# Optimization experiments

Measured on AMD Instinct MI355X. Metric: run time of the kernel, lower is better.

## Reference

```python
import jax, jax.numpy as jnp
import numpy as np

NUM_HEADS = 16
HEAD_DIM = 64
SCALE = 1.0 / np.sqrt(HEAD_DIM).astype(np.float32)


def _clinear(xr, xi, wr, wi):
    # complex matmul: (xr + i xi) @ (wr + i wi)
    yr = jnp.dot(xr, wr) - jnp.dot(xi, wi)
    yi = jnp.dot(xr, wi) + jnp.dot(xi, wr)
    return yr, yi


def setup_inputs() -> dict:
    key = jax.random.key(0)
    ks = jax.random.split(key, 12)
    B, L, S, C = 2, 2048, 2048, 1024
    glorot = 1.0 / np.sqrt(C)
    inp = {
        'inputs_real': jax.random.normal(ks[0], (B, L, C), jnp.float32),
        'inputs_imag': jax.random.normal(ks[1], (B, L, C), jnp.float32),
        'context_real': jax.random.normal(ks[2], (B, S, C), jnp.float32),
        'context_imag': jax.random.normal(ks[3], (B, S, C), jnp.float32),
        'wq_r': jax.random.normal(ks[4], (C, C), jnp.float32) * glorot,
        'wq_i': jax.random.normal(ks[5], (C, C), jnp.float32) * glorot,
        'wk_r': jax.random.normal(ks[6], (C, C), jnp.float32) * glorot,
        'wk_i': jax.random.normal(ks[7], (C, C), jnp.float32) * glorot,
        'wv_r': jax.random.normal(ks[8], (C, C), jnp.float32) * glorot,
        'wv_i': jax.random.normal(ks[9], (C, C), jnp.float32) * glorot,
        'wo_r': jax.random.normal(ks[10], (C, C), jnp.float32) * glorot,
        'wo_i': jax.random.normal(ks[11], (C, C), jnp.float32) * glorot,
        'bo_r': jnp.zeros((C,), jnp.float32),
        'bo_i': jnp.zeros((C,), jnp.float32),
    }
    return inp


def reference(inputs_real, inputs_imag, context_real, context_imag,
              wq_r, wq_i, wk_r, wk_i, wv_r, wv_i, wo_r, wo_i, bo_r, bo_i):
    B, L, C = inputs_real.shape
    S = context_real.shape[1]
    H, D = NUM_HEADS, HEAD_DIM

    qr, qi = _clinear(inputs_real, inputs_imag, wq_r, wq_i)
    kr, ki = _clinear(context_real, context_imag, wk_r, wk_i)
    vr, vi = _clinear(context_real, context_imag, wv_r, wv_i)

    qr = qr.reshape(B, L, H, D); qi = qi.reshape(B, L, H, D)
    kr = kr.reshape(B, S, H, D); ki = ki.reshape(B, S, H, D)
    vr = vr.reshape(B, S, H, D); vi = vi.reshape(B, S, H, D)

    # real part of q . conj-free inner product: qr.kr + qi.ki, scaled
    scores = (jnp.einsum('blhd,bshd->bhls', qr, kr)
              + jnp.einsum('blhd,bshd->bhls', qi, ki)) * SCALE
    attn = jax.nn.softmax(scores, axis=-1)

    out_r = jnp.einsum('bhls,bshd->blhd', attn, vr).reshape(B, L, C)
    out_i = jnp.einsum('bhls,bshd->blhd', attn, vi).reshape(B, L, C)

    yr, yi = _clinear(out_r, out_i, wo_r, wo_i)
    yr = yr + bo_r
    yi = yi + bo_i
    # stack real/imag parts: shape [2, B, L, C]
    return jnp.stack([yr, yi], axis=0)
```

## Files before the change

kernel.cpp:

```cpp
#include <hip/hip_runtime.h>

#define BB 2
#define LQ 2048
#define SK 2048
#define CH 1024
#define NH 16
#define HD 64
#define GK 2048
#define MM 4096
#define ATT_SCALE 0.125f

typedef _Float16 f16x8 __attribute__((ext_vector_type(8)));
typedef float f32x4 __attribute__((ext_vector_type(4)));
typedef unsigned short u16x8 __attribute__((ext_vector_type(8)));

__device__ __forceinline__ unsigned short h2u(_Float16 h) {
    union { _Float16 h; unsigned short u; } v; v.h = h; return v.u;
}
__device__ __forceinline__ void gload16(const _Float16* g, unsigned short* l) {
    __builtin_amdgcn_global_load_lds(
        (const __attribute__((address_space(1))) void*)g,
        (__attribute__((address_space(3))) void*)l, 16, 0, 0);
}

__device__ __forceinline__ float dpp_max16(float x) {
    union { float f; int i; } v, r;
    v.f = x;
    r.i = __builtin_amdgcn_update_dpp(v.i, v.i, 0xB1, 0xF, 0xF, false);
    v.f = fmaxf(v.f, r.f);
    r.i = __builtin_amdgcn_update_dpp(v.i, v.i, 0x4E, 0xF, 0xF, false);
    v.f = fmaxf(v.f, r.f);
    r.i = __builtin_amdgcn_update_dpp(v.i, v.i, 0x141, 0xF, 0xF, false);
    v.f = fmaxf(v.f, r.f);
    r.i = __builtin_amdgcn_update_dpp(v.i, v.i, 0x140, 0xF, 0xF, false);
    v.f = fmaxf(v.f, r.f);
    return v.f;
}

struct PackXEnt { const float* r; const float* i; _Float16* dst; };
struct PackXBatch { PackXEnt e[2]; };

__global__ __launch_bounds__(256) void pack_x_kernel(PackXBatch b)
{
    PackXEnt e = b.e[blockIdx.z];
    const size_t total = (size_t)MM * GK;
    for (size_t idx = (size_t)blockIdx.x * 256 + threadIdx.x; idx < total;
         idx += (size_t)gridDim.x * 256) {
        size_t m = idx >> 11;
        int c = (int)(idx & 2047);
        float v = (c < CH) ? e.r[m * CH + c] : e.i[m * CH + (c - CH)];
        e.dst[idx] = (_Float16)v;
    }
}

struct PackWEnt { const float* a; const float* b; float signb; _Float16* dst; };
struct PackWBatch { PackWEnt e[8]; };

__global__ __launch_bounds__(256) void pack_w_kernel(PackWBatch bt)
{
    PackWEnt e = bt.e[blockIdx.z];
    const int k0 = blockIdx.x * 32;
    const int n0 = blockIdx.y * 32;
    const float* src = (k0 < CH) ? e.a : e.b;
    const float sign = (k0 < CH) ? 1.f : e.signb;
    const int kk = k0 & (CH - 1);

    __shared__ float sT[32][33];
    const int t = threadIdx.x;
    const int tx = t & 31, ty = t >> 5;

    #pragma unroll
    for (int r = 0; r < 4; r++) {
        int kl = ty + r * 8;
        sT[kl][tx] = src[(size_t)(kk + kl) * CH + n0 + tx] * sign;
    }
    __syncthreads();
    #pragma unroll
    for (int r = 0; r < 4; r++) {
        int nl = ty + r * 8;
        e.dst[(size_t)(n0 + nl) * GK + k0 + tx] = (_Float16)sT[tx][nl];
    }
}

struct GemmEnt { const _Float16* A; const _Float16* Bt; void* out;
                 const float* bias; int mode; int part; };
struct GemmBatch { GemmEnt e[6]; };

#define NT   (GK / 32)
#define BUFH 12288

#define SWZ(x) ((x) ^ ((((x) >> 7) & 3) << 4))

__global__ __launch_bounds__(512, 2) void mfma_cgemm(GemmBatch bt)
{
    GemmEnt e = bt.e[blockIdx.z];
    __shared__ unsigned short lds[4 * BUFH];

    const int t    = threadIdx.x;
    const int wave = t >> 6;
    const int lane = t & 63;
    const int lm   = lane & 15;
    const int quad = lane >> 4;
    const int wr   = wave >> 1;
    const int wc   = wave & 1;

    const int m0 = blockIdx.y * 256;
    const int n0 = blockIdx.x * 128;

    int srow[2], scol[2];
    #pragma unroll
    for (int L = 0; L < 2; L++) {
        int p = (L * 512 + t) * 16;
        int q = SWZ(p);
        srow[L] = q >> 6;
        scol[L] = (q >> 1) & 31;
    }

    const _Float16* gA = e.A  + (size_t)m0 * GK;
    const _Float16* gB = e.Bt + (size_t)n0 * GK;

    auto stage = [&](int kt) {
        unsigned short* base = lds + (kt & 3) * BUFH;
        #pragma unroll
        for (int L = 0; L < 2; L++)
            gload16(gA + (size_t)srow[L] * GK + kt * 32 + scol[L],
                    base + (L * 512 + t) * 8);
        gload16(gB + (size_t)srow[0] * GK + kt * 32 + scol[0],
                base + 8192 + t * 8);
    };

    const int qA    = (wr * 64 + lm) * 64 + quad * 16;
    const int physA = SWZ(qA) >> 1;
    const int qB    = (wc * 64 + lm) * 64 + quad * 16;
    const int physB = (SWZ(qB) >> 1) + 8192;

    f32x4 acc[4][4] = {};

    stage(0); stage(1); stage(2);
    asm volatile("s_waitcnt vmcnt(6)" ::: "memory");
    __builtin_amdgcn_s_barrier();

    for (int kt = 0; kt < NT; ++kt) {
        const unsigned short* buf = lds + (kt & 3) * BUFH;
        f16x8 af[4], bf[4];
        #pragma unroll
        for (int i = 0; i < 4; i++)
            af[i] = *(const f16x8*)&buf[physA + i * 512];
        #pragma unroll
        for (int j = 0; j < 4; j++)
            bf[j] = *(const f16x8*)&buf[physB + j * 512];

        if (kt + 3 < NT) stage(kt + 3);

        __builtin_amdgcn_s_barrier();
        asm volatile("s_waitcnt lgkmcnt(0)" ::: "memory");
        __builtin_amdgcn_s_setprio(1);
        #pragma unroll
        for (int i = 0; i < 4; i++)
            #pragma unroll
            for (int j = 0; j < 4; j++)
                acc[i][j] = __builtin_amdgcn_mfma_f32_16x16x32_f16(
                    af[i], bf[j], acc[i][j], 0, 0, 0);
        __builtin_amdgcn_s_setprio(0);

        if (kt < NT - 3)       asm volatile("s_waitcnt vmcnt(6)" ::: "memory");
        else if (kt == NT - 3) asm volatile("s_waitcnt vmcnt(3)" ::: "memory");
        else if (kt == NT - 2) asm volatile("s_waitcnt vmcnt(0)" ::: "memory");
        __builtin_amdgcn_s_barrier();
    }

    const int mode = e.mode, part = e.part;
    #pragma unroll
    for (int j = 0; j < 4; j++) {
        int gcol = n0 + wc * 64 + j * 16 + lm;
        float bv = (mode == 2 && e.bias) ? e.bias[gcol] : 0.f;
        #pragma unroll
        for (int i = 0; i < 4; i++) {
            int growb = m0 + wr * 64 + i * 16 + quad * 4;
            #pragma unroll
            for (int reg = 0; reg < 4; reg++) {
                int grow = growb + reg;
                float v = acc[i][j][reg];
                if (mode == 2) {
                    ((float*)e.out)[(size_t)grow * CH + gcol] = v + bv;
                } else {
                    int b = grow >> 11, l = grow & 2047;
                    int h = gcol >> 6, dd = gcol & 63;
                    size_t off;
                    if (mode == 0)
                        off = (((size_t)(b * NH + h)) * LQ + l) * 128 + part * 64 + dd;
                    else
                        off = (((size_t)(b * NH + h)) * 128 + part * 64 + dd) * SK + l;
                    ((_Float16*)e.out)[off] = (_Float16)v;
                }
            }
        }
    }
}

#define KSTR 136
#define PSTR 72

__global__ __launch_bounds__(256, 2) void attn_mfma(
    const _Float16* __restrict__ Qp, const _Float16* __restrict__ Kp,
    const _Float16* __restrict__ Vt, _Float16* __restrict__ Aattn)
{
    __shared__ unsigned short lds[28288];
    unsigned short* sP = lds;
    unsigned short* sK = lds + 9216;
    unsigned short* sV = lds + 17920;

    const int t    = threadIdx.x;
    const int w    = t >> 6;
    const int lane = t & 63;
    const int lm   = lane & 15;
    const int quad = lane >> 4;

    const int bid = blockIdx.x;
    const int mt  = bid & 15;
    const int h   = (bid >> 4) & 15;
    const int b   = bid >> 8;

    const _Float16* qb = Qp + (((size_t)(b * NH + h)) * LQ + (size_t)mt * 128) * 128;
    const _Float16* kb = Kp + ((size_t)(b * NH + h)) * SK * 128;
    const _Float16* vb = Vt + ((size_t)(b * NH + h)) * 128 * SK;

    #pragma unroll
    for (int p = 0; p < 8; p++) {
        int idx = p * 256 + t;
        int r = idx >> 4, sg = idx & 15;
        *(u16x8*)&lds[r * KSTR + sg * 8] = *(const u16x8*)(qb + (size_t)r * 128 + sg * 8);
    }
    for (int idx = t; idx < 16 * PSTR; idx += 256) {
        sV[128 * PSTR + idx] = 0x3C00;
    }
    __syncthreads();

    f16x8 qf[2][4];
    #pragma unroll
    for (int i = 0; i < 2; i++)
        #pragma unroll
        for (int kk = 0; kk < 4; kk++)
            qf[i][kk] = *(const f16x8*)&lds[(w * 32 + i * 16 + lm) * KSTR + kk * 32 + quad * 8];

    u16x8 kreg[4], vreg[4];
    #pragma unroll
    for (int p = 0; p < 4; p++) {
        int idx = p * 256 + t;
        int r = idx >> 4, sg = idx & 15;
        kreg[p] = *(const u16x8*)(kb + (size_t)r * 128 + sg * 8);
        int rv = idx >> 3, sv = idx & 7;
        vreg[p] = *(const u16x8*)(vb + (size_t)rv * SK + sv * 8);
    }

    f32x4 oacc[2][9] = {};
    float m_st[2][4];
    #pragma unroll
    for (int i = 0; i < 2; i++)
        #pragma unroll
        for (int r = 0; r < 4; r++) m_st[i][r] = -1e30f;

    const float SC2 = ATT_SCALE * 1.44269504f;

    for (int it = 0; it < SK / 64; ++it) {
        __syncthreads();
        #pragma unroll
        for (int p = 0; p < 4; p++) {
            int idx = p * 256 + t;
            int r = idx >> 4, sg = idx & 15;
            *(u16x8*)&sK[r * KSTR + sg * 8] = kreg[p];
            int rv = idx >> 3, sv = idx & 7;
            *(u16x8*)&sV[rv * PSTR + sv * 8] = vreg[p];
        }
        __syncthreads();

        if (it + 1 < SK / 64) {
            int s0n = (it + 1) * 64;
            #pragma unroll
            for (int p = 0; p < 4; p++) {
                int idx = p * 256 + t;
                int r = idx >> 4, sg = idx & 15;
                kreg[p] = *(const u16x8*)(kb + (size_t)(s0n + r) * 128 + sg * 8);
                int rv = idx >> 3, sv = idx & 7;
                vreg[p] = *(const u16x8*)(vb + (size_t)rv * SK + s0n + sv * 8);
            }
        }

        f32x4 sacc[2][4] = {};
        #pragma unroll
        for (int kk = 0; kk < 4; kk++) {
            f16x8 bfr[4];
            #pragma unroll
            for (int j = 0; j < 4; j++)
                bfr[j] = *(const f16x8*)&sK[(j * 16 + lm) * KSTR + kk * 32 + quad * 8];
            #pragma unroll
            for (int i = 0; i < 2; i++)
                #pragma unroll
                for (int j = 0; j < 4; j++)
                    sacc[i][j] = __builtin_amdgcn_mfma_f32_16x16x32_f16(
                        qf[i][kk], bfr[j], sacc[i][j], 0, 0, 0);
        }

        #pragma unroll
        for (int i = 0; i < 2; i++) {
            #pragma unroll
            for (int r = 0; r < 4; r++) {
                float mx = fmaxf(fmaxf(sacc[i][0][r], sacc[i][1][r]),
                                 fmaxf(sacc[i][2][r], sacc[i][3][r]));
                mx = dpp_max16(mx) * SC2;
                float mnew = fmaxf(m_st[i][r], mx);
                float al = exp2f(m_st[i][r] - mnew);
                m_st[i][r] = mnew;
                int prow = (w * 32 + i * 16 + quad * 4 + r) * PSTR;
                #pragma unroll
                for (int j = 0; j < 4; j++) {
                    float p = exp2f(sacc[i][j][r] * SC2 - mnew);
                    sP[prow + j * 16 + lm] = h2u((_Float16)p);
                }
                #pragma unroll
                for (int j2 = 0; j2 < 9; j2++)
                    oacc[i][j2][r] *= al;
            }
        }

        #pragma unroll
        for (int kk = 0; kk < 2; kk++) {
            f16x8 pf[2], vf[9];
            #pragma unroll
            for (int i = 0; i < 2; i++)
                pf[i] = *(const f16x8*)&sP[(w * 32 + i * 16 + lm) * PSTR + kk * 32 + quad * 8];
            #pragma unroll
            for (int j2 = 0; j2 < 9; j2++)
                vf[j2] = *(const f16x8*)&sV[(j2 * 16 + lm) * PSTR + kk * 32 + quad * 8];
            #pragma unroll
            for (int i = 0; i < 2; i++)
                #pragma unroll
                for (int j2 = 0; j2 < 9; j2++)
                    oacc[i][j2] = __builtin_amdgcn_mfma_f32_16x16x32_f16(
                        pf[i], vf[j2], oacc[i][j2], 0, 0, 0);
        }
    }

    #pragma unroll
    for (int i = 0; i < 2; i++) {
        #pragma unroll
        for (int r = 0; r < 4; r++) {
            float inv = 1.f / oacc[i][8][r];
            int ml = w * 32 + i * 16 + quad * 4 + r;
            size_t row = (size_t)b * LQ + (size_t)mt * 128 + ml;
            #pragma unroll
            for (int j2 = 0; j2 < 8; j2++) {
                int d = j2 * 16 + lm;
                int dcol = (d < HD) ? h * HD + d : CH + h * HD + (d - HD);
                Aattn[row * GK + dcol] = (_Float16)(oacc[i][j2][r] * inv);
            }
        }
    }
}

extern "C" void kernel_launch(void* const* d_in, const int* in_sizes, int n_in,
                              void* d_out, int out_size, void* d_ws, size_t ws_size,
                              hipStream_t stream)
{
    const float* in_r = (const float*)d_in[0];
    const float* in_i = (const float*)d_in[1];
    const float* cx_r = (const float*)d_in[2];
    const float* cx_i = (const float*)d_in[3];
    const float* wq_r = (const float*)d_in[4];
    const float* wq_i = (const float*)d_in[5];
    const float* wk_r = (const float*)d_in[6];
    const float* wk_i = (const float*)d_in[7];
    const float* wv_r = (const float*)d_in[8];
    const float* wv_i = (const float*)d_in[9];
    const float* wo_r = (const float*)d_in[10];
    const float* wo_i = (const float*)d_in[11];
    const float* bo_r = (const float*)d_in[12];
    const float* bo_i = (const float*)d_in[13];

    _Float16* ws = (_Float16*)d_ws;
    const size_t A_ELEMS = (size_t)MM * GK;
    const size_t B_ELEMS = (size_t)CH * GK;
    const size_t H_ELEMS = (size_t)BB * NH * LQ * 128;

    _Float16* Ain   = ws;
    _Float16* Aattn = ws;
    _Float16* Actx  = Ain + A_ELEMS;
    _Float16* Bp    = Actx + A_ELEMS;
    _Float16* Qp    = Bp + 8 * B_ELEMS;
    _Float16* Kp    = Qp + H_ELEMS;
    _Float16* Vt    = Kp + H_ELEMS;

    _Float16* Bq_r = Bp + 0 * B_ELEMS;
    _Float16* Bq_i = Bp + 1 * B_ELEMS;
    _Float16* Bk_r = Bp + 2 * B_ELEMS;
    _Float16* Bk_i = Bp + 3 * B_ELEMS;
    _Float16* Bv_r = Bp + 4 * B_ELEMS;
    _Float16* Bv_i = Bp + 5 * B_ELEMS;
    _Float16* Bo_r = Bp + 6 * B_ELEMS;
    _Float16* Bo_i = Bp + 7 * B_ELEMS;

    float* out = (float*)d_out;
    float* yr = out;
    float* yi = out + (size_t)MM * CH;

    PackXBatch px;
    px.e[0] = { in_r, in_i, Ain  };
    px.e[1] = { cx_r, cx_i, Actx };
    pack_x_kernel<<<dim3(4096, 1, 2), 256, 0, stream>>>(px);

    PackWBatch pw;
    pw.e[0] = { wq_r, wq_i, -1.f, Bq_r };
    pw.e[1] = { wq_i, wq_r,  1.f, Bq_i };
    pw.e[2] = { wk_r, wk_i, -1.f, Bk_r };
    pw.e[3] = { wk_i, wk_r,  1.f, Bk_i };
    pw.e[4] = { wv_r, wv_i, -1.f, Bv_r };
    pw.e[5] = { wv_i, wv_r,  1.f, Bv_i };
    pw.e[6] = { wo_r, wo_i, -1.f, Bo_r };
    pw.e[7] = { wo_i, wo_r,  1.f, Bo_i };
    pack_w_kernel<<<dim3(GK / 32, CH / 32, 8), 256, 0, stream>>>(pw);

    GemmBatch gq;
    gq.e[0] = { Ain,  Bq_r, Qp, nullptr, 0, 0 };
    gq.e[1] = { Ain,  Bq_i, Qp, nullptr, 0, 1 };
    gq.e[2] = { Actx, Bk_r, Kp, nullptr, 0, 0 };
    gq.e[3] = { Actx, Bk_i, Kp, nullptr, 0, 1 };
    gq.e[4] = { Actx, Bv_r, Vt, nullptr, 1, 0 };
    gq.e[5] = { Actx, Bv_i, Vt, nullptr, 1, 1 };
    mfma_cgemm<<<dim3(CH / 128, MM / 256, 6), 512, 0, stream>>>(gq);

    attn_mfma<<<dim3(BB * NH * (LQ / 128)), 256, 0, stream>>>(Qp, Kp, Vt, Aattn);

    GemmBatch go;
    go.e[0] = { Aattn, Bo_r, yr, bo_r, 2, 0 };
    go.e[1] = { Aattn, Bo_i, yi, bo_i, 2, 1 };
    for (int z = 2; z < 6; z++) go.e[z] = go.e[0];
    mfma_cgemm<<<dim3(CH / 128, MM / 256, 2), 512, 0, stream>>>(go);
}
```

Baseline: 486.7 us.

## Swizzle attention LDS layout, remap block order, and add lazy softmax rescaling

Padded LDS strides for Q, K, V and P are replaced by an XOR swizzle. This shrinks the shared buffer and is meant to avoid bank conflicts on the MFMA fragment reads. Block indices are remapped so consecutive workgroups spread across heads/batches, presumably to balance work across XCDs and their caches. The online softmax now rescales the output accumulators only when the running max grows by more than 8 in the log2 domain. This skips most rescale multiplies, at the risk of fp16 P values reaching up to 2^8 before normalization.

```diff
diff --git a/kernel.cpp b/kernel.cpp
--- a/kernel.cpp
+++ b/kernel.cpp
@@ -35,6 +35,10 @@
     r.i = __builtin_amdgcn_update_dpp(v.i, v.i, 0x140, 0xF, 0xF, false);
     v.f = fmaxf(v.f, r.f);
     return v.f;
+}
+
+__device__ __forceinline__ int swzi(int row, int colh, int ldh) {
+    return row * ldh + (colh ^ ((row & 7) << 3));
 }
 
 struct PackXEnt { const float* r; const float* i; _Float16* dst; };
@@ -198,17 +202,14 @@
     }
 }
 
-#define KSTR 136
-#define PSTR 72
-
 __global__ __launch_bounds__(256, 2) void attn_mfma(
     const _Float16* __restrict__ Qp, const _Float16* __restrict__ Kp,
     const _Float16* __restrict__ Vt, _Float16* __restrict__ Aattn)
 {
-    __shared__ unsigned short lds[28288];
+    __shared__ unsigned short lds[25600];
     unsigned short* sP = lds;
-    unsigned short* sK = lds + 9216;
-    unsigned short* sV = lds + 17920;
+    unsigned short* sK = lds + 8192;
+    unsigned short* sV = lds + 16384;
 
     const int t    = threadIdx.x;
     const int w    = t >> 6;
@@ -216,7 +217,8 @@
     const int lm   = lane & 15;
     const int quad = lane >> 4;
 
-    const int bid = blockIdx.x;
+    const int bx  = blockIdx.x;
+    const int bid = (bx & 7) * 64 + (bx >> 3);
     const int mt  = bid & 15;
     const int h   = (bid >> 4) & 15;
     const int b   = bid >> 8;
@@ -229,10 +231,12 @@
     for (int p = 0; p < 8; p++) {
         int idx = p * 256 + t;
         int r = idx >> 4, sg = idx & 15;
-        *(u16x8*)&lds[r * KSTR + sg * 8] = *(const u16x8*)(qb + (size_t)r * 128 + sg * 8);
-    }
-    for (int idx = t; idx < 16 * PSTR; idx += 256) {
-        sV[128 * PSTR + idx] = 0x3C00;
+        *(u16x8*)&lds[swzi(r, sg * 8, 128)] = *(const u16x8*)(qb + (size_t)r * 128 + sg * 8);
+    }
+    for (int idx = t; idx < 16 * 64; idx += 256) {
+        int row = 128 + (idx >> 6);
+        int col = idx & 63;
+        sV[row * 64 + (col ^ ((row & 7) << 3))] = 0x3C00;
     }
     __syncthreads();
 
@@ -241,7 +245,7 @@
     for (int i = 0; i < 2; i++)
         #pragma unroll
         for (int kk = 0; kk < 4; kk++)
-            qf[i][kk] = *(const f16x8*)&lds[(w * 32 + i * 16 + lm) * KSTR + kk * 32 + quad * 8];
+            qf[i][kk] = *(const f16x8*)&lds[swzi(w * 32 + i * 16 + lm, kk * 32 + quad * 8, 128)];
 
     u16x8 kreg[4], vreg[4];
     #pragma unroll
@@ -268,9 +272,9 @@
         for (int p = 0; p < 4; p++) {
             int idx = p * 256 + t;
             int r = idx >> 4, sg = idx & 15;
-            *(u16x8*)&sK[r * KSTR + sg * 8] = kreg[p];
+            *(u16x8*)&sK[swzi(r, sg * 8, 128)] = kreg[p];
             int rv = idx >> 3, sv = idx & 7;
-            *(u16x8*)&sV[rv * PSTR + sv * 8] = vreg[p];
+            *(u16x8*)&sV[swzi(rv, sv * 8, 64)] = vreg[p];
         }
         __syncthreads();
 
@@ -292,7 +296,7 @@
             f16x8 bfr[4];
             #pragma unroll
             for (int j = 0; j < 4; j++)
-                bfr[j] = *(const f16x8*)&sK[(j * 16 + lm) * KSTR + kk * 32 + quad * 8];
+                bfr[j] = *(const f16x8*)&sK[swzi(j * 16 + lm, kk * 32 + quad * 8, 128)];
             #pragma unroll
             for (int i = 0; i < 2; i++)
                 #pragma unroll
@@ -308,18 +312,20 @@
                 float mx = fmaxf(fmaxf(sacc[i][0][r], sacc[i][1][r]),
                                  fmaxf(sacc[i][2][r], sacc[i][3][r]));
                 mx = dpp_max16(mx) * SC2;
-                float mnew = fmaxf(m_st[i][r], mx);
-                float al = exp2f(m_st[i][r] - mnew);
-                m_st[i][r] = mnew;
-                int prow = (w * 32 + i * 16 + quad * 4 + r) * PSTR;
+                if (mx > m_st[i][r] + 8.0f) {
+                    float al = exp2f(m_st[i][r] - mx);
+                    m_st[i][r] = mx;
+                    #pragma unroll
+                    for (int j2 = 0; j2 < 9; j2++)
+                        oacc[i][j2][r] *= al;
+                }
+                float mcur = m_st[i][r];
+                int rowp = w * 32 + i * 16 + quad * 4 + r;
                 #pragma unroll
                 for (int j = 0; j < 4; j++) {
-                    float p = exp2f(sacc[i][j][r] * SC2 - mnew);
-                    sP[prow + j * 16 + lm] = h2u((_Float16)p);
+                    float p = exp2f(sacc[i][j][r] * SC2 - mcur);
+                    sP[swzi(rowp, j * 16 + lm, 64)] = h2u((_Float16)p);
                 }
-                #pragma unroll
-                for (int j2 = 0; j2 < 9; j2++)
-                    oacc[i][j2][r] *= al;
             }
         }
 
@@ -328,10 +334,10 @@
             f16x8 pf[2], vf[9];
             #pragma unroll
             for (int i = 0; i < 2; i++)
-                pf[i] = *(const f16x8*)&sP[(w * 32 + i * 16 + lm) * PSTR + kk * 32 + quad * 8];
+                pf[i] = *(const f16x8*)&sP[swzi(w * 32 + i * 16 + lm, kk * 32 + quad * 8, 64)];
             #pragma unroll
             for (int j2 = 0; j2 < 9; j2++)
-                vf[j2] = *(const f16x8*)&sV[(j2 * 16 + lm) * PSTR + kk * 32 + quad * 8];
+                vf[j2] = *(const f16x8*)&sV[swzi(j2 * 16 + lm, kk * 32 + quad * 8, 64)];
             #pragma unroll
             for (int i = 0; i < 2; i++)
                 #pragma unroll
```

Measured after the change: 513.6 us. +5.5%, slower.
